# Performance work log

Measured on AMD Instinct MI355X. Metric: run time of the kernel, lower is better.

Reference implementation:

```python
import jax, jax.numpy as jnp
import numpy as np

C = 343.0                      # wave speed
OMEGA = 2.0 * np.pi * 1000.0   # angular frequency
K2 = (C / OMEGA) ** 2          # coefficient on u in the (as-written) residual

N_POINTS = 262144
HIDDEN = 256


def _mlp_point(p, W1, b1, W2, b2, W3, b3, W4, b4):
    # p: (3,) -> scalar u(x,y,z); tanh MLP stand-in for model_estimation
    h = jnp.tanh(p @ W1 + b1)
    h = jnp.tanh(h @ W2 + b2)
    h = jnp.tanh(h @ W3 + b3)
    return (h @ W4 + b4)[0]


def setup_inputs() -> dict:
    key = jax.random.key(0)
    ks = jax.random.split(key, 5)

    def init_w(k, fan_in, fan_out):
        return jax.random.normal(k, (fan_in, fan_out), dtype=jnp.float32) / np.sqrt(fan_in).astype(np.float32)

    inputs = jax.random.normal(ks[0], (N_POINTS, 3), dtype=jnp.float32)
    W1 = init_w(ks[1], 3, HIDDEN)
    W2 = init_w(ks[2], HIDDEN, HIDDEN)
    W3 = init_w(ks[3], HIDDEN, HIDDEN)
    W4 = init_w(ks[4], HIDDEN, 1)
    z = lambda n: jnp.zeros((n,), dtype=jnp.float32)
    return {
        "inputs": inputs,
        "W1": W1, "b1": z(HIDDEN),
        "W2": W2, "b2": z(HIDDEN),
        "W3": W3, "b3": z(HIDDEN),
        "W4": W4, "b4": z(1),
    }


def reference(inputs, W1, b1, W2, b2, W3, b3, W4, b4):
    # Per-point scalar field u(p); Laplacian = trace of the 3x3 Hessian.
    def u_point(p):
        return _mlp_point(p, W1, b1, W2, b2, W3, b3, W4, b4)

    u = jax.vmap(u_point)(inputs)                       # [N]
    hess = jax.vmap(jax.hessian(u_point))(inputs)       # [N, 3, 3]
    laplace_u = hess[:, 0, 0] + hess[:, 1, 1] + hess[:, 2, 2]  # [N]

    pde_residual = laplace_u + K2 * u
    return jnp.mean(jnp.abs(pde_residual) ** 2)
```

## Files before the change

### kernel.cpp

```cpp
#include <hip/hip_runtime.h>
#include <math.h>

#define HID 256
#define PTS 16
#define NSTR 5
#define ROWS (NSTR*PTS)
#define PITCH 272

typedef __fp16  fp16x2 __attribute__((ext_vector_type(2)));
typedef _Float16 half8  __attribute__((ext_vector_type(8)));
typedef float   floatx4 __attribute__((ext_vector_type(4)));

constexpr double PI_D = 3.14159265358979323846;
constexpr float K2F = (float)((343.0/(2.0*PI_D*1000.0))*(343.0/(2.0*PI_D*1000.0)));

union H2U { fp16x2 h; unsigned int u; };
__device__ __forceinline__ unsigned int pk(float a, float b) {
  H2U t; t.h = __builtin_amdgcn_cvt_pkrtz(a, b); return t.u;
}

__device__ __forceinline__ float tanh_fast(float z) {
  float e = __builtin_amdgcn_exp2f(z * 2.8853900817779268f);
  return 1.0f - 2.0f * __builtin_amdgcn_rcpf(e + 1.0f);
}

__global__ void pack_kernel(const float* __restrict__ W2, const float* __restrict__ W3,
                            _Float16* __restrict__ out) {
  int t = blockIdx.x * blockDim.x + threadIdx.x;
  int l    = t >> 13;
  int rem  = t & 8191;
  int kc   = rem >> 10;
  int nt   = (rem >> 6) & 15;
  int lane = rem & 63;
  const float* W = l ? W3 : W2;
  int k0 = kc*32 + ((lane >> 4) << 3);
  int n  = (nt >> 2)*64 + (lane & 15)*4 + (nt & 3);
  _Float16* o = out + (size_t)t * 8;
  #pragma unroll
  for (int j = 0; j < 8; ++j)
    o[j] = (_Float16)W[(size_t)(k0 + j)*HID + n];
}

__global__ __launch_bounds__(256, 3) void helm_kernel(
    const float* __restrict__ inputs,
    const float* __restrict__ W1, const float* __restrict__ b1,
    const float* __restrict__ b2, const float* __restrict__ b3,
    const float* __restrict__ W4, const float* __restrict__ b4,
    const _Float16* __restrict__ Wpack,
    float* __restrict__ part)
{
  __shared__ __align__(16) _Float16 X[ROWS][PITCH];

  const int tid  = threadIdx.x;
  const int lane = tid & 63;
  const int wave = tid >> 6;
  const int m    = lane & 15;
  const int q    = lane >> 4;

  const int pbase = blockIdx.x * PTS;

  {
    const int p  = tid >> 4;
    const int c0 = (tid & 15) * 16;
    const float x0 = inputs[(size_t)(pbase + p)*3 + 0];
    const float x1 = inputs[(size_t)(pbase + p)*3 + 1];
    const float x2 = inputs[(size_t)(pbase + p)*3 + 2];
    #pragma unroll
    for (int ch = 0; ch < 2; ++ch) {
      float v[NSTR][8];
      #pragma unroll
      for (int jj = 0; jj < 2; ++jj) {
        const int n = c0 + ch*8 + jj*4;
        floatx4 w0 = *(const floatx4*)&W1[0*HID + n];
        floatx4 w1 = *(const floatx4*)&W1[1*HID + n];
        floatx4 w2 = *(const floatx4*)&W1[2*HID + n];
        floatx4 bn = *(const floatx4*)&b1[n];
        #pragma unroll
        for (int e = 0; e < 4; ++e) {
          float z  = fmaf(x2, w2[e], fmaf(x1, w1[e], fmaf(x0, w0[e], bn[e])));
          float a  = tanh_fast(z);
          float dd = 1.0f - a*a;
          float wsq = fmaf(w0[e], w0[e], fmaf(w1[e], w1[e], w2[e]*w2[e]));
          v[0][jj*4+e] = a;
          v[1][jj*4+e] = dd*w0[e];
          v[2][jj*4+e] = dd*w1[e];
          v[3][jj*4+e] = dd*w2[e];
          v[4][jj*4+e] = -2.0f*a*dd*wsq;
        }
      }
      #pragma unroll
      for (int s = 0; s < NSTR; ++s) {
        uint4 u;
        u.x = pk(v[s][0], v[s][1]); u.y = pk(v[s][2], v[s][3]);
        u.z = pk(v[s][4], v[s][5]); u.w = pk(v[s][6], v[s][7]);
        *(uint4*)&X[s*PTS + p][c0 + ch*8] = u;
      }
    }
  }
  __syncthreads();

  const int colbase = wave*64 + m*4;

  auto kloop = [&](const _Float16* __restrict__ Wp, floatx4 (&acc)[NSTR][4]) {
    const _Float16* wb = Wp + (((size_t)(wave*4)*64 + lane) << 3);
    #pragma unroll
    for (int kc = 0; kc < 8; ++kc) {
      half8 bfrag[4];
      #pragma unroll
      for (int c = 0; c < 4; ++c)
        bfrag[c] = *(const half8*)(wb + (size_t)kc*8192 + c*512);
      half8 afrag[NSTR];
      #pragma unroll
      for (int s = 0; s < NSTR; ++s)
        afrag[s] = *(const half8*)(&X[s*PTS + m][kc*32 + q*8]);
      #pragma unroll
      for (int s = 0; s < NSTR; ++s)
        #pragma unroll
        for (int c = 0; c < 4; ++c)
          acc[s][c] = __builtin_amdgcn_mfma_f32_16x16x32_f16(afrag[s], bfrag[c], acc[s][c], 0, 0, 0);
    }
  };

  {
    floatx4 acc[NSTR][4];
    #pragma unroll
    for (int s = 0; s < NSTR; ++s)
      #pragma unroll
      for (int c = 0; c < 4; ++c)
        acc[s][c] = (floatx4){0.0f, 0.0f, 0.0f, 0.0f};
    kloop(Wpack, acc);
    __syncthreads();

    floatx4 bv = *(const floatx4*)&b2[colbase];
    #pragma unroll
    for (int r = 0; r < 4; ++r) {
      const int p = q*4 + r;
      float va[4], vg0[4], vg1[4], vg2[4], vT[4];
      #pragma unroll
      for (int c = 0; c < 4; ++c) {
        float z  = acc[0][c][r] + bv[c];
        float a  = tanh_fast(z);
        float dd = 1.0f - a*a;
        float z0 = acc[1][c][r], z1 = acc[2][c][r], z2 = acc[3][c][r];
        float zpp = acc[4][c][r];
        float s2 = fmaf(z0, z0, fmaf(z1, z1, z2*z2));
        va[c]  = a;
        vg0[c] = dd*z0; vg1[c] = dd*z1; vg2[c] = dd*z2;
        vT[c]  = fmaf(dd, zpp, -2.0f*a*dd*s2);
      }
      uint2 u;
      u.x = pk(va[0],va[1]);   u.y = pk(va[2],va[3]);   *(uint2*)&X[0*PTS + p][colbase] = u;
      u.x = pk(vg0[0],vg0[1]); u.y = pk(vg0[2],vg0[3]); *(uint2*)&X[1*PTS + p][colbase] = u;
      u.x = pk(vg1[0],vg1[1]); u.y = pk(vg1[2],vg1[3]); *(uint2*)&X[2*PTS + p][colbase] = u;
      u.x = pk(vg2[0],vg2[1]); u.y = pk(vg2[2],vg2[3]); *(uint2*)&X[3*PTS + p][colbase] = u;
      u.x = pk(vT[0],vT[1]);   u.y = pk(vT[2],vT[3]);   *(uint2*)&X[4*PTS + p][colbase] = u;
    }
    __syncthreads();
  }

  {
    floatx4 acc[NSTR][4];
    #pragma unroll
    for (int s = 0; s < NSTR; ++s)
      #pragma unroll
      for (int c = 0; c < 4; ++c)
        acc[s][c] = (floatx4){0.0f, 0.0f, 0.0f, 0.0f};
    kloop(Wpack + 65536, acc);
    __syncthreads();

    floatx4 bv = *(const floatx4*)&b3[colbase];
    floatx4 w4 = *(const floatx4*)&W4[colbase];
    float su[4] = {0,0,0,0}, st[4] = {0,0,0,0};
    #pragma unroll
    for (int r = 0; r < 4; ++r)
      #pragma unroll
      for (int c = 0; c < 4; ++c) {
        float z  = acc[0][c][r] + bv[c];
        float a  = tanh_fast(z);
        float dd = 1.0f - a*a;
        float z0 = acc[1][c][r], z1 = acc[2][c][r], z2 = acc[3][c][r];
        float zpp = acc[4][c][r];
        float s2 = fmaf(z0, z0, fmaf(z1, z1, z2*z2));
        float T  = fmaf(dd, zpp, -2.0f*a*dd*s2);
        su[r] = fmaf(a, w4[c], su[r]);
        st[r] = fmaf(T, w4[c], st[r]);
      }

    #pragma unroll
    for (int off = 8; off >= 1; off >>= 1)
      #pragma unroll
      for (int r = 0; r < 4; ++r) {
        su[r] += __shfl_down(su[r], off);
        st[r] += __shfl_down(st[r], off);
      }
    float* S = (float*)X;
    if (m == 0) {
      #pragma unroll
      for (int r = 0; r < 4; ++r) {
        S[(q*4 + r)*8 + wave]     = su[r];
        S[(q*4 + r)*8 + 4 + wave] = st[r];
      }
    }
  }
  __syncthreads();

  if (wave == 0) {
    const float* S = (const float*)X;
    int pidx = lane >> 2, w = lane & 3;
    float suc = S[pidx*8 + w];
    float stc = S[pidx*8 + 4 + w];
    suc += __shfl_down(suc, 1); suc += __shfl_down(suc, 2);
    stc += __shfl_down(stc, 1); stc += __shfl_down(stc, 2);
    float sq = 0.0f;
    if ((lane & 3) == 0) {
      float u   = suc + b4[0];
      float res = fmaf(K2F, u, stc);
      sq = res * res;
    }
    sq += __shfl_down(sq, 4); sq += __shfl_down(sq, 8);
    sq += __shfl_down(sq, 16); sq += __shfl_down(sq, 32);
    if (lane == 0) part[blockIdx.x] = sq;
  }
}

__global__ void reduce_kernel(const float* __restrict__ part, float* __restrict__ out,
                              int nblk, float scale) {
  float s = 0.0f;
  for (int i = threadIdx.x; i < (nblk >> 2); i += 256) {
    floatx4 v = *(const floatx4*)&part[i << 2];
    s += (v[0] + v[1]) + (v[2] + v[3]);
  }
  #pragma unroll
  for (int off = 32; off; off >>= 1) s += __shfl_down(s, off);
  __shared__ float sm[4];
  if ((threadIdx.x & 63) == 0) sm[threadIdx.x >> 6] = s;
  __syncthreads();
  if (threadIdx.x == 0) out[0] = ((sm[0] + sm[1]) + (sm[2] + sm[3])) * scale;
}

extern "C" void kernel_launch(void* const* d_in, const int* in_sizes, int n_in,
                              void* d_out, int out_size, void* d_ws, size_t ws_size,
                              hipStream_t stream) {
  const float* inputs = (const float*)d_in[0];
  const float* W1 = (const float*)d_in[1];
  const float* b1 = (const float*)d_in[2];
  const float* W2 = (const float*)d_in[3];
  const float* b2 = (const float*)d_in[4];
  const float* W3 = (const float*)d_in[5];
  const float* b3 = (const float*)d_in[6];
  const float* W4 = (const float*)d_in[7];
  const float* b4 = (const float*)d_in[8];
  float* out = (float*)d_out;

  _Float16* wp   = (_Float16*)d_ws;
  float*    part = (float*)((char*)d_ws + 2*65536*2);

  int N    = in_sizes[0] / 3;
  int nblk = N / PTS;

  pack_kernel<<<64, 256, 0, stream>>>(W2, W3, wp);
  helm_kernel<<<nblk, 256, 0, stream>>>(inputs, W1, b1, b2, b3, W4, b4, wp, part);
  reduce_kernel<<<1, 256, 0, stream>>>(part, out, nblk, 1.0f / (float)N);
}
```

Before: 408.3 us.

## Stagger first-wave blocks, raise MFMA priority, fold biases and precompute W1 norms

Blocks in the first three groups of 256 now sleep for a staggered time at start, so waves fall out of phase and their MFMA and ALU phases overlap across the CU. The MFMA burst in the k-loop runs at raised wave priority. Biases b2/b3 are loaded into the accumulator start value instead of being added after the matmul. The per-column squared norm of W1 is precomputed in an extra pack block and loaded instead of recomputed per point. This adds a small workspace buffer and an explicit startup delay for early blocks.

```diff
diff --git a/kernel.cpp b/kernel.cpp
--- a/kernel.cpp
+++ b/kernel.cpp
@@ -25,7 +25,14 @@
 }
 
 __global__ void pack_kernel(const float* __restrict__ W2, const float* __restrict__ W3,
-                            _Float16* __restrict__ out) {
+                            const float* __restrict__ W1,
+                            _Float16* __restrict__ out, float* __restrict__ wsq) {
+  if (blockIdx.x == 64) {
+    int n = threadIdx.x;
+    float w0 = W1[0*HID + n], w1 = W1[1*HID + n], w2 = W1[2*HID + n];
+    wsq[n] = fmaf(w0, w0, fmaf(w1, w1, w2*w2));
+    return;
+  }
   int t = blockIdx.x * blockDim.x + threadIdx.x;
   int l    = t >> 13;
   int rem  = t & 8191;
@@ -47,6 +54,7 @@
     const float* __restrict__ b2, const float* __restrict__ b3,
     const float* __restrict__ W4, const float* __restrict__ b4,
     const _Float16* __restrict__ Wpack,
+    const float* __restrict__ wsqv,
     float* __restrict__ part)
 {
   __shared__ __align__(16) _Float16 X[ROWS][PITCH];
@@ -56,6 +64,12 @@
   const int wave = tid >> 6;
   const int m    = lane & 15;
   const int q    = lane >> 4;
+
+  if (blockIdx.x < 768) {
+    int ph = blockIdx.x >> 8;
+    if (ph > 0) __builtin_amdgcn_s_sleep(70);
+    if (ph > 1) __builtin_amdgcn_s_sleep(70);
+  }
 
   const int pbase = blockIdx.x * PTS;
 
@@ -75,17 +89,17 @@
         floatx4 w1 = *(const floatx4*)&W1[1*HID + n];
         floatx4 w2 = *(const floatx4*)&W1[2*HID + n];
         floatx4 bn = *(const floatx4*)&b1[n];
+        floatx4 ws = *(const floatx4*)&wsqv[n];
         #pragma unroll
         for (int e = 0; e < 4; ++e) {
           float z  = fmaf(x2, w2[e], fmaf(x1, w1[e], fmaf(x0, w0[e], bn[e])));
           float a  = tanh_fast(z);
           float dd = 1.0f - a*a;
-          float wsq = fmaf(w0[e], w0[e], fmaf(w1[e], w1[e], w2[e]*w2[e]));
           v[0][jj*4+e] = a;
           v[1][jj*4+e] = dd*w0[e];
           v[2][jj*4+e] = dd*w1[e];
           v[3][jj*4+e] = dd*w2[e];
-          v[4][jj*4+e] = -2.0f*a*dd*wsq;
+          v[4][jj*4+e] = -2.0f*a*dd*ws[e];
         }
       }
       #pragma unroll
@@ -113,32 +127,36 @@
       #pragma unroll
       for (int s = 0; s < NSTR; ++s)
         afrag[s] = *(const half8*)(&X[s*PTS + m][kc*32 + q*8]);
+      __builtin_amdgcn_s_setprio(1);
       #pragma unroll
       for (int s = 0; s < NSTR; ++s)
         #pragma unroll
         for (int c = 0; c < 4; ++c)
           acc[s][c] = __builtin_amdgcn_mfma_f32_16x16x32_f16(afrag[s], bfrag[c], acc[s][c], 0, 0, 0);
+      __builtin_amdgcn_s_setprio(0);
     }
   };
 
   {
+    floatx4 bv = *(const floatx4*)&b2[colbase];
     floatx4 acc[NSTR][4];
     #pragma unroll
-    for (int s = 0; s < NSTR; ++s)
-      #pragma unroll
-      for (int c = 0; c < 4; ++c)
+    for (int c = 0; c < 4; ++c) {
+      acc[0][c] = (floatx4){bv[c], bv[c], bv[c], bv[c]};
+      #pragma unroll
+      for (int s = 1; s < NSTR; ++s)
         acc[s][c] = (floatx4){0.0f, 0.0f, 0.0f, 0.0f};
+    }
     kloop(Wpack, acc);
     __syncthreads();
 
-    floatx4 bv = *(const floatx4*)&b2[colbase];
     #pragma unroll
     for (int r = 0; r < 4; ++r) {
       const int p = q*4 + r;
       float va[4], vg0[4], vg1[4], vg2[4], vT[4];
       #pragma unroll
       for (int c = 0; c < 4; ++c) {
-        float z  = acc[0][c][r] + bv[c];
+        float z  = acc[0][c][r];
         float a  = tanh_fast(z);
         float dd = 1.0f - a*a;
         float z0 = acc[1][c][r], z1 = acc[2][c][r], z2 = acc[3][c][r];
@@ -159,23 +177,25 @@
   }
 
   {
+    floatx4 bv = *(const floatx4*)&b3[colbase];
     floatx4 acc[NSTR][4];
     #pragma unroll
-    for (int s = 0; s < NSTR; ++s)
-      #pragma unroll
-      for (int c = 0; c < 4; ++c)
+    for (int c = 0; c < 4; ++c) {
+      acc[0][c] = (floatx4){bv[c], bv[c], bv[c], bv[c]};
+      #pragma unroll
+      for (int s = 1; s < NSTR; ++s)
         acc[s][c] = (floatx4){0.0f, 0.0f, 0.0f, 0.0f};
+    }
     kloop(Wpack + 65536, acc);
     __syncthreads();
 
-    floatx4 bv = *(const floatx4*)&b3[colbase];
     floatx4 w4 = *(const floatx4*)&W4[colbase];
     float su[4] = {0,0,0,0}, st[4] = {0,0,0,0};
     #pragma unroll
     for (int r = 0; r < 4; ++r)
       #pragma unroll
       for (int c = 0; c < 4; ++c) {
-        float z  = acc[0][c][r] + bv[c];
+        float z  = acc[0][c][r];
         float a  = tanh_fast(z);
         float dd = 1.0f - a*a;
         float z0 = acc[1][c][r], z1 = acc[2][c][r], z2 = acc[3][c][r];
@@ -254,11 +274,12 @@
 
   _Float16* wp   = (_Float16*)d_ws;
   float*    part = (float*)((char*)d_ws + 2*65536*2);
+  float*    wsq  = (float*)((char*)d_ws + 2*65536*2 + 65536);
 
   int N    = in_sizes[0] / 3;
   int nblk = N / PTS;
 
-  pack_kernel<<<64, 256, 0, stream>>>(W2, W3, wp);
-  helm_kernel<<<nblk, 256, 0, stream>>>(inputs, W1, b1, b2, b3, W4, b4, wp, part);
+  pack_kernel<<<65, 256, 0, stream>>>(W2, W3, W1, wp, wsq);
+  helm_kernel<<<nblk, 256, 0, stream>>>(inputs, W1, b1, b2, b3, W4, b4, wp, wsq, part);
   reduce_kernel<<<1, 256, 0, stream>>>(part, out, nblk, 1.0f / (float)N);
 }
```

New measurement: 419.0 us. 2.6% more time.
